# Kernel optimization log

Hardware: AMD Instinct MI355X
Metric: run time of the kernel (lower is better)

Reference implementation:

```python
import jax, jax.numpy as jnp
import numpy as np

# Detector / geometry constants (mirrors DRR.__init__ kwargs)
SDD = 1020.0           # source-to-detector distance (mm)
H, W = 160, 160        # detector pixels
DELX, DELY = 2.5, 2.5  # pixel pitch (mm)
X0, Y0 = 0.0, 0.0
VOL = 256              # CT volume is VOL^3 voxels
SPACING = 1.5          # voxel spacing (mm)
EPS = 1e-8


def setup_inputs() -> dict:
    key = jax.random.key(0)
    density = jax.random.uniform(key, (VOL, VOL, VOL), dtype=jnp.float32)
    # rigid camera pose: rotate the C-arm about x; isocenter at the world origin
    th = 0.2
    c, s = np.cos(th), np.sin(th)
    R = np.array([[1, 0, 0], [0, c, -s], [0, s, c]], dtype=np.float32)
    t = R @ np.array([0.0, 0.0, -SDD / 2.0], dtype=np.float32)  # source 510mm from isocenter
    pose = np.eye(4, dtype=np.float32)
    pose[:3, :3], pose[:3, 3] = R, t
    # voxel -> world affine: isotropic spacing, volume centered at the origin
    affine = np.eye(4, dtype=np.float32)
    affine[:3, :3] *= SPACING
    affine[:3, 3] = -SPACING * VOL / 2.0
    affine_inv = jnp.asarray(np.linalg.inv(affine).astype(np.float32))
    return {"density": density, "pose": jnp.asarray(pose)[None], "affine_inv": affine_inv}


def _detector_rays():
    # camera frame: X-ray source at the origin, detector plane at z = SDD
    xs = (jnp.arange(W, dtype=jnp.float32) - (W - 1) / 2.0) * DELX + X0
    ys = (jnp.arange(H, dtype=jnp.float32) - (H - 1) / 2.0) * DELY + Y0
    tx, ty = jnp.meshgrid(xs, ys, indexing="xy")
    targets = jnp.stack([tx.ravel(), ty.ravel(), jnp.full((H * W,), SDD, jnp.float32)], -1)
    source = jnp.zeros((1, 3), jnp.float32)
    return source, targets  # [1,3], [H*W,3]


def _pose_apply(pose, pts):  # pose [B,4,4], pts [N,3] -> [B,N,3]
    return jnp.einsum("bij,nj->bni", pose[:, :3, :3], pts) + pose[:, None, :3, 3]


def _affine_apply(A, pts):  # A [4,4], pts [B,N,3] -> [B,N,3]
    return jnp.einsum("ij,bnj->bni", A[:3, :3], pts) + A[:3, 3]


def _siddon(density, src, tgt, raylen):
    # Exact Siddon line integral. src [B,1,3], tgt [B,N,3] in voxel coords.
    dims = jnp.asarray(density.shape, jnp.float32)
    sd = tgt - src                                   # ray directions [B,N,3]
    sd_safe = jnp.where(jnp.abs(sd) < EPS, EPS, sd)  # avoid div-by-zero
    # parametric entry/exit of the segment with the volume bounding box
    a0 = (0.0 - src) / sd_safe
    a1 = (dims - src) / sd_safe
    amin = jnp.maximum(jnp.max(jnp.minimum(a0, a1), -1), 0.0)  # [B,N]
    amax = jnp.minimum(jnp.min(jnp.maximum(a0, a1), -1), 1.0)
    amax = jnp.maximum(amax, amin)
    # intersections with every axis-aligned voxel plane, sorted per ray
    planes = [
        (jnp.arange(n + 1, dtype=jnp.float32)[None, None, :] - src[..., i:i + 1]) / sd_safe[..., i:i + 1]
        for i, n in enumerate(density.shape)
    ]
    alphas = jnp.sort(jnp.concatenate(planes, -1), -1)          # [B,N,P], P = sum(n_i+1)
    # clamping collapses out-of-volume intersections to zero-length intervals
    alphas = jnp.clip(alphas, amin[..., None], amax[..., None])
    steps = jnp.diff(alphas, axis=-1)                           # [B,N,P-1] segment lengths (in alpha)
    amid = 0.5 * (alphas[..., :-1] + alphas[..., 1:])           # segment midpoints
    # voxel index at each midpoint, computed per axis to avoid a [B,N,P,3] stack
    idx = tuple(
        jnp.clip(jnp.floor(src[..., i:i + 1] + amid * sd[..., i:i + 1]).astype(jnp.int32), 0, density.shape[i] - 1)
        for i in range(3)
    )
    vox = density[idx[0], idx[1], idx[2]]                       # irregular gather [B,N,P-1]
    return jnp.sum(vox * steps, -1) * raylen                    # [B,N]


def reference(density, pose, affine_inv):
    src_c, tgt_c = _detector_rays()
    src_w = _pose_apply(pose, src_c)                 # [B,1,3]
    tgt_w = _pose_apply(pose, tgt_c)                 # [B,N,3]
    raylen = jnp.linalg.norm(tgt_w - src_w, axis=-1)  # img = (target-source).norm(dim=-1)
    src_v = _affine_apply(affine_inv, src_w)          # world -> voxel
    tgt_v = _affine_apply(affine_inv, tgt_w)
    drr = _siddon(density, src_v, tgt_v, raylen)
    return drr.reshape(pose.shape[0], 1, H, W)        # img.view(len(pose), -1, H, W)
```

## Files before the change

kernel.cpp:

```cpp
#include <hip/hip_runtime.h>

static constexpr float F_SDD = 1020.0f;
static constexpr int   DH = 160, DW = 160;
static constexpr float DELX = 2.5f, DELY = 2.5f;
static constexpr int   VOL = 256;
static constexpr int   NRAY = DH * DW;
static constexpr int   TILES_X = DW / 8;
static constexpr int   TILES_Y = DH / 8;
static constexpr int   NTILE = TILES_X * TILES_Y;
static constexpr int   CHUNKS = 8;
static constexpr int   SUBS = 4;
static constexpr int   KB = 4;
static constexpr float EPS = 1e-8f;

extern "C" __global__ void zero_out_kernel(float* __restrict__ out, int n) {
    int i = blockIdx.x * blockDim.x + threadIdx.x;
    if (i < n) out[i] = 0.0f;
}

extern "C" __global__ void __launch_bounds__(256)
drr_siddon_kernel(const float* __restrict__ density,
                  const float* __restrict__ pose,
                  const float* __restrict__ ainv,
                  float* __restrict__ out)
{
    __shared__ float red[256];

    int chunk = blockIdx.x & (CHUNKS - 1);
    int tile  = blockIdx.x >> 3;
    int tx = tile % TILES_X, ty = tile / TILES_X;

    int tid  = threadIdx.x;
    int sub  = tid >> 6;
    int lane = tid & 63;

    int px = tx * 8 + (lane & 7);
    int py = ty * 8 + (lane >> 3);
    int ray = py * DW + px;

    float xs = ((float)px - (DW - 1) * 0.5f) * DELX;
    float ys = ((float)py - (DH - 1) * 0.5f) * DELY;

    float R00 = pose[0], R01 = pose[1], R02 = pose[2],  t0 = pose[3];
    float R10 = pose[4], R11 = pose[5], R12 = pose[6],  t1 = pose[7];
    float R20 = pose[8], R21 = pose[9], R22 = pose[10], t2 = pose[11];

    float sw0 = t0, sw1 = t1, sw2 = t2;
    float tw0 = R00 * xs + R01 * ys + R02 * F_SDD + t0;
    float tw1 = R10 * xs + R11 * ys + R12 * F_SDD + t1;
    float tw2 = R20 * xs + R21 * ys + R22 * F_SDD + t2;

    float dw0 = tw0 - sw0, dw1 = tw1 - sw1, dw2 = tw2 - sw2;
    float raylen = sqrtf(dw0 * dw0 + dw1 * dw1 + dw2 * dw2);

    float A00 = ainv[0], A01 = ainv[1], A02 = ainv[2],  A03 = ainv[3];
    float A10 = ainv[4], A11 = ainv[5], A12 = ainv[6],  A13 = ainv[7];
    float A20 = ainv[8], A21 = ainv[9], A22 = ainv[10], A23 = ainv[11];

    float s0 = A00 * sw0 + A01 * sw1 + A02 * sw2 + A03;
    float s1 = A10 * sw0 + A11 * sw1 + A12 * sw2 + A13;
    float s2 = A20 * sw0 + A21 * sw1 + A22 * sw2 + A23;
    float g0 = A00 * tw0 + A01 * tw1 + A02 * tw2 + A03;
    float g1 = A10 * tw0 + A11 * tw1 + A12 * tw2 + A13;
    float g2 = A20 * tw0 + A21 * tw1 + A22 * tw2 + A23;

    float sd0 = g0 - s0, sd1 = g1 - s1, sd2 = g2 - s2;
    float e0 = (fabsf(sd0) < EPS) ? EPS : sd0;
    float e1 = (fabsf(sd1) < EPS) ? EPS : sd1;
    float e2 = (fabsf(sd2) < EPS) ? EPS : sd2;
    float inv0 = 1.0f / e0, inv1 = 1.0f / e1, inv2 = 1.0f / e2;

    float lo0 = (0.0f - s0) * inv0, hi0 = ((float)VOL - s0) * inv0;
    float lo1 = (0.0f - s1) * inv1, hi1 = ((float)VOL - s1) * inv1;
    float lo2 = (0.0f - s2) * inv2, hi2 = ((float)VOL - s2) * inv2;
    float amin = fmaxf(fmaxf(fminf(lo0, hi0), fminf(lo1, hi1)), fminf(lo2, hi2));
    amin = fmaxf(amin, 0.0f);
    float amax = fminf(fminf(fmaxf(lo0, hi0), fmaxf(lo1, hi1)), fmaxf(lo2, hi2));
    amax = fminf(amax, 1.0f);
    amax = fmaxf(amax, amin);

    float arange  = amax - amin;
    float c_start = amin + arange * ((float)chunk * (1.0f / CHUNKS));
    float c_end   = (chunk == CHUNKS - 1) ? amax
                    : amin + arange * ((float)(chunk + 1) * (1.0f / CHUNKS));
    float crange  = c_end - c_start;
    float a_start = c_start + crange * ((float)sub * (1.0f / SUBS));
    float a_end   = (sub == SUBS - 1) ? c_end
                    : c_start + crange * ((float)(sub + 1) * (1.0f / SUBS));

    float ax0, ax1, ax2, da0, da1, da2;
    if (fabsf(sd0) < EPS) { ax0 = 3.0e38f; da0 = 0.0f; }
    else {
        float p = s0 + a_start * sd0;
        float k = (sd0 > 0.0f) ? (floorf(p) + 1.0f) : (ceilf(p) - 1.0f);
        ax0 = (k - s0) * inv0; da0 = fabsf(inv0);
    }
    if (fabsf(sd1) < EPS) { ax1 = 3.0e38f; da1 = 0.0f; }
    else {
        float p = s1 + a_start * sd1;
        float k = (sd1 > 0.0f) ? (floorf(p) + 1.0f) : (ceilf(p) - 1.0f);
        ax1 = (k - s1) * inv1; da1 = fabsf(inv1);
    }
    if (fabsf(sd2) < EPS) { ax2 = 3.0e38f; da2 = 0.0f; }
    else {
        float p = s2 + a_start * sd2;
        float k = (sd2 > 0.0f) ? (floorf(p) + 1.0f) : (ceilf(p) - 1.0f);
        ax2 = (k - s2) * inv2; da2 = fabsf(inv2);
    }

    float acc = 0.0f;
    float alpha = a_start;
    while (alpha < a_end) {
        float seg[KB];
        float val[KB];
#pragma unroll
        for (int k = 0; k < KB; ++k) {
            float m     = fminf(fminf(ax0, ax1), ax2);
            float astop = fminf(m, a_end);
            float amid  = 0.5f * (alpha + astop);
            seg[k] = fmaxf(astop - alpha, 0.0f);
            float c0 = truncf(fminf(fmaxf(fmaf(amid, sd0, s0), 0.0f), 255.0f));
            float c1 = truncf(fminf(fmaxf(fmaf(amid, sd1, s1), 0.0f), 255.0f));
            float c2 = truncf(fminf(fmaxf(fmaf(amid, sd2, s2), 0.0f), 255.0f));
            int idx = (int)fmaf(c0, 65536.0f, fmaf(c1, 256.0f, c2));
            val[k] = density[idx];
            if (ax0 <= m) ax0 += da0;
            if (ax1 <= m) ax1 += da1;
            if (ax2 <= m) ax2 += da2;
            alpha = m;
        }
#pragma unroll
        for (int k = 0; k < KB; ++k) acc = fmaf(val[k], seg[k], acc);
    }

    red[tid] = acc;
    __syncthreads();
    if (tid < 64) {
        float total = red[tid] + red[tid + 64] + red[tid + 128] + red[tid + 192];
        atomicAdd(&out[ray], total * raylen);
    }
}

extern "C" void kernel_launch(void* const* d_in, const int* in_sizes, int n_in,
                              void* d_out, int out_size, void* d_ws, size_t ws_size,
                              hipStream_t stream) {
    const float* density = (const float*)d_in[0];
    const float* pose    = (const float*)d_in[1];
    const float* ainv    = (const float*)d_in[2];
    float* out = (float*)d_out;

    hipLaunchKernelGGL(zero_out_kernel, dim3((NRAY + 255) / 256), dim3(256), 0,
                       stream, out, NRAY);

    dim3 block(256);
    dim3 grid(NTILE * CHUNKS);
    hipLaunchKernelGGL(drr_siddon_kernel, grid, block, 0, stream,
                       density, pose, ainv, out);
}
```

Baseline: 35.17 us.

## Stage per-tile voxel tube into LDS and march rays from shared memory

Each block now covers a 16x8 ray tile with 128 threads. Every thread marches its whole chunk sequentially in four stages instead of four waves splitting the segment. Per stage the block finds the voxel bounding box of all its rays with wave shuffles, loads that box into LDS with float4 loads if it fits a 22x16x16 cap, and reads voxels from LDS during the Siddon march, with a fallback to global gathers when the box is too large. The goal is to replace scattered global gathers with coalesced loads that are reused across rays. In exchange it adds barriers and a large LDS footprint that lowers occupancy, and per-ray parallelism drops fourfold.

```diff
diff --git a/kernel.cpp b/kernel.cpp
--- a/kernel.cpp
+++ b/kernel.cpp
@@ -5,12 +5,15 @@
 static constexpr float DELX = 2.5f, DELY = 2.5f;
 static constexpr int   VOL = 256;
 static constexpr int   NRAY = DH * DW;
-static constexpr int   TILES_X = DW / 8;
-static constexpr int   TILES_Y = DH / 8;
+static constexpr int   PX_T = 16, PY_T = 8;
+static constexpr int   TILES_X = DW / PX_T;
+static constexpr int   TILES_Y = DH / PY_T;
 static constexpr int   NTILE = TILES_X * TILES_Y;
 static constexpr int   CHUNKS = 8;
-static constexpr int   SUBS = 4;
+static constexpr int   NSTG = 4;
 static constexpr int   KB = 4;
+static constexpr int   CAP_N0 = 22;
+static constexpr int   PLANE = 260;
 static constexpr float EPS = 1e-8f;
 
 extern "C" __global__ void zero_out_kernel(float* __restrict__ out, int n) {
@@ -18,24 +21,22 @@
     if (i < n) out[i] = 0.0f;
 }
 
-extern "C" __global__ void __launch_bounds__(256)
+extern "C" __global__ void __launch_bounds__(128)
 drr_siddon_kernel(const float* __restrict__ density,
                   const float* __restrict__ pose,
                   const float* __restrict__ ainv,
                   float* __restrict__ out)
 {
-    __shared__ float red[256];
+    __shared__ float tube[CAP_N0 * PLANE];
+    __shared__ float sb[2][6];
 
     int chunk = blockIdx.x & (CHUNKS - 1);
     int tile  = blockIdx.x >> 3;
     int tx = tile % TILES_X, ty = tile / TILES_X;
 
-    int tid  = threadIdx.x;
-    int sub  = tid >> 6;
-    int lane = tid & 63;
-
-    int px = tx * 8 + (lane & 7);
-    int py = ty * 8 + (lane >> 3);
+    int tid = threadIdx.x;
+    int px = tx * PX_T + (tid & 15);
+    int py = ty * PY_T + (tid >> 4);
     int ray = py * DW + px;
 
     float xs = ((float)px - (DW - 1) * 0.5f) * DELX;
@@ -84,61 +85,126 @@
     float c_end   = (chunk == CHUNKS - 1) ? amax
                     : amin + arange * ((float)(chunk + 1) * (1.0f / CHUNKS));
     float crange  = c_end - c_start;
-    float a_start = c_start + crange * ((float)sub * (1.0f / SUBS));
-    float a_end   = (sub == SUBS - 1) ? c_end
-                    : c_start + crange * ((float)(sub + 1) * (1.0f / SUBS));
-
-    float ax0, ax1, ax2, da0, da1, da2;
-    if (fabsf(sd0) < EPS) { ax0 = 3.0e38f; da0 = 0.0f; }
-    else {
-        float p = s0 + a_start * sd0;
-        float k = (sd0 > 0.0f) ? (floorf(p) + 1.0f) : (ceilf(p) - 1.0f);
-        ax0 = (k - s0) * inv0; da0 = fabsf(inv0);
+
+    float da0 = fabsf(inv0), da1 = fabsf(inv1), da2 = fabsf(inv2);
+
+    float acc = 0.0f;
+
+    for (int stg = 0; stg < NSTG; ++stg) {
+        float a0 = (stg == 0) ? c_start
+                   : c_start + crange * ((float)stg * (1.0f / NSTG));
+        float a1 = (stg == NSTG - 1) ? c_end
+                   : c_start + crange * ((float)(stg + 1) * (1.0f / NSTG));
+
+        float qA0 = truncf(fminf(fmaxf(fmaf(a0, sd0, s0), 0.0f), 255.0f));
+        float qA1 = truncf(fminf(fmaxf(fmaf(a0, sd1, s1), 0.0f), 255.0f));
+        float qA2 = truncf(fminf(fmaxf(fmaf(a0, sd2, s2), 0.0f), 255.0f));
+        float qB0 = truncf(fminf(fmaxf(fmaf(a1, sd0, s0), 0.0f), 255.0f));
+        float qB1 = truncf(fminf(fmaxf(fmaf(a1, sd1, s1), 0.0f), 255.0f));
+        float qB2 = truncf(fminf(fmaxf(fmaf(a1, sd2, s2), 0.0f), 255.0f));
+        float l0 = fminf(qA0, qB0), h0 = fmaxf(qA0, qB0);
+        float l1 = fminf(qA1, qB1), h1 = fmaxf(qA1, qB1);
+        float l2 = fminf(qA2, qB2), h2 = fmaxf(qA2, qB2);
+        for (int msk = 1; msk < 64; msk <<= 1) {
+            l0 = fminf(l0, __shfl_xor(l0, msk));  h0 = fmaxf(h0, __shfl_xor(h0, msk));
+            l1 = fminf(l1, __shfl_xor(l1, msk));  h1 = fmaxf(h1, __shfl_xor(h1, msk));
+            l2 = fminf(l2, __shfl_xor(l2, msk));  h2 = fmaxf(h2, __shfl_xor(h2, msk));
+        }
+        if ((tid & 63) == 0) {
+            int wv = tid >> 6;
+            sb[wv][0] = l0; sb[wv][1] = h0; sb[wv][2] = l1;
+            sb[wv][3] = h1; sb[wv][4] = l2; sb[wv][5] = h2;
+        }
+        __syncthreads();
+        int b0  = (int)fminf(sb[0][0], sb[1][0]);
+        int t0_ = (int)fmaxf(sb[0][1], sb[1][1]);
+        int b1  = (int)fminf(sb[0][2], sb[1][2]);
+        int t1_ = (int)fmaxf(sb[0][3], sb[1][3]);
+        int b2  = (int)fminf(sb[0][4], sb[1][4]);
+        int t2_ = (int)fmaxf(sb[0][5], sb[1][5]);
+        int b2a = b2 & ~3;
+        int n0 = t0_ - b0 + 1;
+        bool fits = (n0 <= CAP_N0) && (t1_ - b1 <= 15) && (t2_ - b2a <= 15);
+
+        float ax0, ax1, ax2;
+        if (fabsf(sd0) < EPS) ax0 = 3.0e38f;
+        else { float p = s0 + a0 * sd0;
+               float kk = (sd0 > 0.0f) ? (floorf(p) + 1.0f) : (ceilf(p) - 1.0f);
+               ax0 = (kk - s0) * inv0; }
+        if (fabsf(sd1) < EPS) ax1 = 3.0e38f;
+        else { float p = s1 + a0 * sd1;
+               float kk = (sd1 > 0.0f) ? (floorf(p) + 1.0f) : (ceilf(p) - 1.0f);
+               ax1 = (kk - s1) * inv1; }
+        if (fabsf(sd2) < EPS) ax2 = 3.0e38f;
+        else { float p = s2 + a0 * sd2;
+               float kk = (sd2 > 0.0f) ? (floorf(p) + 1.0f) : (ceilf(p) - 1.0f);
+               ax2 = (kk - s2) * inv2; }
+
+        if (fits) {
+            int nq  = n0 << 6;
+            int sk1 = t1_ - b1;
+            for (int e = tid; e < nq; e += 128) {
+                int q0 = e >> 6, rem = e & 63, q1 = rem >> 2, qc = (rem & 3) << 2;
+                if (q1 <= sk1) {
+                    int gz = min(b2a + qc, 252);
+                    const float4 v = *(const float4*)(density +
+                        (((b0 + q0) << 16) | ((b1 + q1) << 8) | gz));
+                    *(float4*)(tube + (q0 * PLANE + (q1 << 4) + qc)) = v;
+                }
+            }
+            __syncthreads();
+
+            float Kf = (float)(b0 * PLANE + (b1 << 4) + b2a);
+            float alpha = a0;
+            while (alpha < a1) {
+                float seg[KB]; float val[KB];
+#pragma unroll
+                for (int k = 0; k < KB; ++k) {
+                    float m    = fminf(fminf(ax0, ax1), ax2);
+                    float as_  = fminf(m, a1);
+                    float amid = fminf(0.5f * (alpha + as_), a1);
+                    seg[k] = fmaxf(as_ - alpha, 0.0f);
+                    float c0 = truncf(fminf(fmaxf(fmaf(amid, sd0, s0), 0.0f), 255.0f));
+                    float c1 = truncf(fminf(fmaxf(fmaf(amid, sd1, s1), 0.0f), 255.0f));
+                    float c2 = truncf(fminf(fmaxf(fmaf(amid, sd2, s2), 0.0f), 255.0f));
+                    int li = (int)(fmaf(c0, (float)PLANE, fmaf(c1, 16.0f, c2)) - Kf);
+                    val[k] = tube[li];
+                    if (ax0 <= m) ax0 += da0;
+                    if (ax1 <= m) ax1 += da1;
+                    if (ax2 <= m) ax2 += da2;
+                    alpha = m;
+                }
+#pragma unroll
+                for (int k = 0; k < KB; ++k) acc = fmaf(val[k], seg[k], acc);
+            }
+        } else {
+            float alpha = a0;
+            while (alpha < a1) {
+                float seg[KB]; float val[KB];
+#pragma unroll
+                for (int k = 0; k < KB; ++k) {
+                    float m    = fminf(fminf(ax0, ax1), ax2);
+                    float as_  = fminf(m, a1);
+                    float amid = fminf(0.5f * (alpha + as_), a1);
+                    seg[k] = fmaxf(as_ - alpha, 0.0f);
+                    float c0 = truncf(fminf(fmaxf(fmaf(amid, sd0, s0), 0.0f), 255.0f));
+                    float c1 = truncf(fminf(fmaxf(fmaf(amid, sd1, s1), 0.0f), 255.0f));
+                    float c2 = truncf(fminf(fmaxf(fmaf(amid, sd2, s2), 0.0f), 255.0f));
+                    int gi = (int)fmaf(c0, 65536.0f, fmaf(c1, 256.0f, c2));
+                    val[k] = density[gi];
+                    if (ax0 <= m) ax0 += da0;
+                    if (ax1 <= m) ax1 += da1;
+                    if (ax2 <= m) ax2 += da2;
+                    alpha = m;
+                }
+#pragma unroll
+                for (int k = 0; k < KB; ++k) acc = fmaf(val[k], seg[k], acc);
+            }
+        }
+        __syncthreads();
     }
-    if (fabsf(sd1) < EPS) { ax1 = 3.0e38f; da1 = 0.0f; }
-    else {
-        float p = s1 + a_start * sd1;
-        float k = (sd1 > 0.0f) ? (floorf(p) + 1.0f) : (ceilf(p) - 1.0f);
-        ax1 = (k - s1) * inv1; da1 = fabsf(inv1);
-    }
-    if (fabsf(sd2) < EPS) { ax2 = 3.0e38f; da2 = 0.0f; }
-    else {
-        float p = s2 + a_start * sd2;
-        float k = (sd2 > 0.0f) ? (floorf(p) + 1.0f) : (ceilf(p) - 1.0f);
-        ax2 = (k - s2) * inv2; da2 = fabsf(inv2);
-    }
-
-    float acc = 0.0f;
-    float alpha = a_start;
-    while (alpha < a_end) {
-        float seg[KB];
-        float val[KB];
-#pragma unroll
-        for (int k = 0; k < KB; ++k) {
-            float m     = fminf(fminf(ax0, ax1), ax2);
-            float astop = fminf(m, a_end);
-            float amid  = 0.5f * (alpha + astop);
-            seg[k] = fmaxf(astop - alpha, 0.0f);
-            float c0 = truncf(fminf(fmaxf(fmaf(amid, sd0, s0), 0.0f), 255.0f));
-            float c1 = truncf(fminf(fmaxf(fmaf(amid, sd1, s1), 0.0f), 255.0f));
-            float c2 = truncf(fminf(fmaxf(fmaf(amid, sd2, s2), 0.0f), 255.0f));
-            int idx = (int)fmaf(c0, 65536.0f, fmaf(c1, 256.0f, c2));
-            val[k] = density[idx];
-            if (ax0 <= m) ax0 += da0;
-            if (ax1 <= m) ax1 += da1;
-            if (ax2 <= m) ax2 += da2;
-            alpha = m;
-        }
-#pragma unroll
-        for (int k = 0; k < KB; ++k) acc = fmaf(val[k], seg[k], acc);
-    }
-
-    red[tid] = acc;
-    __syncthreads();
-    if (tid < 64) {
-        float total = red[tid] + red[tid + 64] + red[tid + 128] + red[tid + 192];
-        atomicAdd(&out[ray], total * raylen);
-    }
+
+    atomicAdd(&out[ray], acc * raylen);
 }
 
 extern "C" void kernel_launch(void* const* d_in, const int* in_sizes, int n_in,
@@ -152,7 +218,7 @@
     hipLaunchKernelGGL(zero_out_kernel, dim3((NRAY + 255) / 256), dim3(256), 0,
                        stream, out, NRAY);
 
-    dim3 block(256);
+    dim3 block(128);
     dim3 grid(NTILE * CHUNKS);
     hipLaunchKernelGGL(drr_siddon_kernel, grid, block, 0, stream,
                        density, pose, ainv, out);
```

After: 41.60 us. 1.18x slower.
